# Performance work log

Hardware: AMD Instinct MI355X
Metric: run time of the kernel (lower is better)

## Reference

```python
import jax, jax.numpy as jnp
import numpy as np

N = 100000
E = 3200000
IN_DIM = 128
OUT_DIM = 64


def setup_inputs() -> dict:
    key = jax.random.key(0)
    k1, k2, k3, k4, k5, k6 = jax.random.split(key, 6)
    x = jax.random.normal(k1, (N, IN_DIM), dtype=jnp.float32)
    edge_index = jax.random.randint(k2, (2, E), 0, N, dtype=jnp.int64)
    edge_weight = jax.random.uniform(k3, (E,), dtype=jnp.float32)
    # Learned params: Linear weight (in->out, no bias), attention vectors a_src/a_tgt
    limit_w = float(np.sqrt(1.0 / IN_DIM))
    W = jax.random.uniform(k4, (IN_DIM, OUT_DIM), minval=-limit_w, maxval=limit_w, dtype=jnp.float32)
    # xavier_uniform for (out_dim, 1) parameters
    limit_a = float(np.sqrt(6.0 / (OUT_DIM + 1)))
    a_src = jax.random.uniform(k5, (OUT_DIM,), minval=-limit_a, maxval=limit_a, dtype=jnp.float32)
    a_tgt = jax.random.uniform(k6, (OUT_DIM,), minval=-limit_a, maxval=limit_a, dtype=jnp.float32)
    return {"x": x, "edge_index": edge_index, "edge_weight": edge_weight,
            "W": W, "a_src": a_src, "a_tgt": a_tgt}


def reference(x, edge_index, edge_weight, W, a_src, a_tgt):
    n = x.shape[0]
    h = x @ W  # (N, out_dim)
    src, tgt = edge_index[0], edge_index[1]
    # per-node attention logits, gathered per edge
    hs = h @ a_src  # (N,)
    ht = h @ a_tgt  # (N,)
    e = jax.nn.leaky_relu(hs[src] + ht[tgt], negative_slope=0.2)  # (E,)
    e = e * edge_weight
    # segment softmax over incoming edges of each target node
    e_max = jax.ops.segment_max(e, tgt, num_segments=n)  # (N,), -inf for isolated nodes
    e_exp = jnp.exp(e - e_max[tgt])  # (E,)
    e_sum = jax.ops.segment_sum(e_exp, tgt, num_segments=n)  # (N,)
    alpha = e_exp / (e_sum[tgt] + 1e-10)  # (E,)
    # weighted scatter-add aggregation
    out = jax.ops.segment_sum(alpha[:, None] * h[src], tgt, num_segments=n)  # (N, out_dim)
    return out
```

## Files before the change

kernel.cpp:

```cpp
#include <hip/hip_runtime.h>


#define IN_DIM 128
#define OUT_DIM 64
#define LNODES 64
#define MAXBKT 512
#define BKN 256
#define SEPT 8
#define SCHUNK (1024 * SEPT)
#define CAP 9216

__device__ __forceinline__ unsigned short f2bf(float f) {
    unsigned u = __float_as_uint(f);
    return (unsigned short)((u + 0x7FFFu + ((u >> 16) & 1u)) >> 16);
}
__device__ __forceinline__ float bf2f(unsigned short u) {
    return __uint_as_float((unsigned)u << 16);
}

__device__ __forceinline__ float expg(float d) {
    return __expf(fmaxf(d, -80.f));
}

__global__ __launch_bounds__(512) void k_linear(
    const float* __restrict__ x, const float* __restrict__ W,
    const float* __restrict__ a_src, const float* __restrict__ a_tgt,
    unsigned short* __restrict__ hh, float* __restrict__ hs,
    float* __restrict__ ht, int n)
{
    __shared__ float ws_W[IN_DIM][OUT_DIM];
    __shared__ float xs[LNODES][IN_DIM + 4];
    const int tid   = threadIdx.x;
    const int node0 = blockIdx.x * LNODES;

    {
        const float4* Wsrc = (const float4*)W;
        float4* Wdst = (float4*)&ws_W[0][0];
        #pragma unroll
        for (int i = 0; i < 4; ++i) Wdst[tid + 512 * i] = Wsrc[tid + 512 * i];
    }
    {
        int nrows = n - node0; if (nrows > LNODES) nrows = LNODES;
        for (int i = tid; i < nrows * 32; i += 512) {
            int r = i >> 5, c4 = i & 31;
            float4 v = ((const float4*)(x + (size_t)(node0 + r) * IN_DIM))[c4];
            *(float4*)&xs[r][c4 * 4] = v;
        }
    }
    __syncthreads();

    const int lane16 = tid & 15;
    const int mrow   = tid >> 4;
    float4 acc[2];
    acc[0] = make_float4(0.f, 0.f, 0.f, 0.f);
    acc[1] = make_float4(0.f, 0.f, 0.f, 0.f);

    #pragma unroll 2
    for (int k = 0; k < IN_DIM; k += 4) {
        float4 w0 = *(const float4*)&ws_W[k + 0][lane16 * 4];
        float4 w1 = *(const float4*)&ws_W[k + 1][lane16 * 4];
        float4 w2 = *(const float4*)&ws_W[k + 2][lane16 * 4];
        float4 w3 = *(const float4*)&ws_W[k + 3][lane16 * 4];
        #pragma unroll
        for (int u = 0; u < 2; ++u) {
            float4 xv = *(const float4*)&xs[mrow + 32 * u][k];
            acc[u].x += w0.x * xv.x + w1.x * xv.y + w2.x * xv.z + w3.x * xv.w;
            acc[u].y += w0.y * xv.x + w1.y * xv.y + w2.y * xv.z + w3.y * xv.w;
            acc[u].z += w0.z * xv.x + w1.z * xv.y + w2.z * xv.z + w3.z * xv.w;
            acc[u].w += w0.w * xv.x + w1.w * xv.y + w2.w * xv.z + w3.w * xv.w;
        }
    }

    const float4 as = ((const float4*)a_src)[lane16];
    const float4 at = ((const float4*)a_tgt)[lane16];
    #pragma unroll
    for (int u = 0; u < 2; ++u) {
        int node = node0 + mrow + 32 * u;
        float ps = acc[u].x * as.x + acc[u].y * as.y + acc[u].z * as.z + acc[u].w * as.w;
        float pt = acc[u].x * at.x + acc[u].y * at.y + acc[u].z * at.z + acc[u].w * at.w;
        #pragma unroll
        for (int off = 8; off; off >>= 1) {
            ps += __shfl_xor(ps, off);
            pt += __shfl_xor(pt, off);
        }
        if (node < n) {
            ushort4 hv;
            hv.x = f2bf(acc[u].x); hv.y = f2bf(acc[u].y);
            hv.z = f2bf(acc[u].z); hv.w = f2bf(acc[u].w);
            ((ushort4*)(hh + (size_t)node * OUT_DIM))[lane16] = hv;
            if (lane16 == 0) { hs[node] = ps; ht[node] = pt; }
        }
    }
}

__global__ __launch_bounds__(1024) void k_count(
    const int* __restrict__ tgt, int* __restrict__ histT,
    int ecount, int nbkt, int nsb)
{
    __shared__ int h[MAXBKT];
    const int tid = threadIdx.x;
    const int e0  = blockIdx.x * SCHUNK;
    for (int i = tid; i < nbkt; i += 1024) h[i] = 0;
    __syncthreads();
    #pragma unroll
    for (int k = 0; k < SEPT; ++k) {
        int j = e0 + k * 1024 + tid;
        if (j < ecount) atomicAdd(&h[tgt[j] >> 8], 1);
    }
    __syncthreads();
    for (int i = tid; i < nbkt; i += 1024) histT[i * nsb + blockIdx.x] = h[i];
}

__global__ __launch_bounds__(512) void k_colscan(
    int* __restrict__ histT, int* __restrict__ bfill, int nsb)
{
    __shared__ int lds[512];
    const int bkt = blockIdx.x;
    const int tid = threadIdx.x;
    int v = (tid < nsb) ? histT[bkt * nsb + tid] : 0;
    lds[tid] = v;
    __syncthreads();
    for (int off = 1; off < 512; off <<= 1) {
        int u = (tid >= off) ? lds[tid - off] : 0;
        __syncthreads();
        lds[tid] += u;
        __syncthreads();
    }
    int excl = lds[tid] - v;
    if (tid < nsb) histT[bkt * nsb + tid] = bkt * CAP + excl;
    if (tid == 511) bfill[bkt] = bkt * CAP + lds[511];
}

__global__ __launch_bounds__(1024) void k_scat(
    const int* __restrict__ src, const int* __restrict__ tgt,
    const float* __restrict__ ew, const float* __restrict__ hs,
    const float* __restrict__ ht, const int* __restrict__ histT,
    float2* __restrict__ ecoarse, int ecount, int nbkt, int nsb)
{
    __shared__ int h[MAXBKT];
    __shared__ int base[MAXBKT];
    const int tid = threadIdx.x;
    const int e0  = blockIdx.x * SCHUNK;

    for (int i = tid; i < nbkt; i += 1024) {
        h[i] = 0;
        base[i] = histT[i * nsb + blockIdx.x];
    }

    unsigned kreg[SEPT]; int breg[SEPT]; float wreg[SEPT];
    #pragma unroll
    for (int k = 0; k < SEPT; ++k) {
        int j = e0 + k * 1024 + tid;
        bool valid = j < ecount;
        int s = valid ? src[j] : 0;
        int t = valid ? tgt[j] : 0;
        wreg[k] = valid ? ew[j] : 0.f;
        kreg[k] = ((unsigned)s << 8) | ((unsigned)t & 255u);
        breg[k] = t >> 8;
    }
    float hsr[SEPT], htr[SEPT];
    #pragma unroll
    for (int k = 0; k < SEPT; ++k) hsr[k] = hs[kreg[k] >> 8];
    #pragma unroll
    for (int k = 0; k < SEPT; ++k) htr[k] = ht[(breg[k] << 8) | (int)(kreg[k] & 255u)];

    __syncthreads();

    int rank[SEPT];
    #pragma unroll
    for (int k = 0; k < SEPT; ++k) {
        int j = e0 + k * 1024 + tid;
        if (j < ecount) rank[k] = atomicAdd(&h[breg[k]], 1);
    }

    #pragma unroll
    for (int k = 0; k < SEPT; ++k) {
        int j = e0 + k * 1024 + tid;
        if (j < ecount) {
            float v = hsr[k] + htr[k];
            v = (v > 0.f) ? v : 0.2f * v;
            v *= wreg[k];
            ecoarse[base[breg[k]] + rank[k]] = make_float2(__uint_as_float(kreg[k]), v);
        }
    }
}

__global__ __launch_bounds__(1024, 8) void k_bucket(
    const int* __restrict__ bfill, const float2* __restrict__ ecoarse,
    const unsigned short* __restrict__ hh, float* __restrict__ out, int n)
{
    __shared__ float2 recs[CAP];
    __shared__ int   cnt[BKN];
    __shared__ int   pos0[BKN];
    __shared__ int   fill[BKN];
    __shared__ float mf[BKN];
    __shared__ float rden[BKN];

    const int tid   = threadIdx.x;
    const int bkt   = blockIdx.x;
    const int base  = bkt * CAP;
    const int node0 = bkt << 8;
    const int mcnt  = bfill[bkt] - base;

    for (int i = tid; i < BKN; i += 1024) cnt[i] = 0;
    __syncthreads();

    for (int j = tid; j < mcnt; j += 1024) {
        unsigned k = __float_as_uint(ecoarse[base + j].x);
        atomicAdd(&cnt[k & 255u], 1);
    }
    __syncthreads();

    if (tid < BKN) pos0[tid] = cnt[tid];
    __syncthreads();
    for (int off = 1; off < BKN; off <<= 1) {
        int u = 0;
        if (tid < BKN && tid >= off) u = pos0[tid - off];
        __syncthreads();
        if (tid < BKN) pos0[tid] += u;
        __syncthreads();
    }
    if (tid < BKN) fill[tid] = pos0[tid] - cnt[tid];
    __syncthreads();
    if (tid < BKN) pos0[tid] = fill[tid];
    __syncthreads();

    for (int j = tid; j < mcnt; j += 1024) {
        float2 e = ecoarse[base + j];
        unsigned k = __float_as_uint(e.x);
        int p = atomicAdd(&fill[k & 255u], 1);
        recs[p] = e;
    }
    __syncthreads();

    {
        const int G   = tid >> 4;
        const int l16 = tid & 15;
        #pragma unroll
        for (int r = 0; r < 4; ++r) {
            int tl = G + 64 * r;
            int s0 = pos0[tl], c = cnt[tl];
            float m = -INFINITY, s = 0.f;
            for (int j = l16; j < c; j += 16) {
                float v = recs[s0 + j].y;
                float nm = fmaxf(m, v);
                s = s * expg(m - nm) + expg(v - nm);
                m = nm;
            }
            #pragma unroll
            for (int off = 8; off; off >>= 1) {
                float mo = __shfl_xor(m, off);
                float so = __shfl_xor(s, off);
                float nm = fmaxf(m, mo);
                s = s * expg(m - nm) + so * expg(mo - nm);
                m = nm;
            }
            if (l16 == 0) { mf[tl] = m; rden[tl] = 1.f / (s + 1e-10f); }
        }
    }
    __syncthreads();

    const int lane = tid & 63;
    const int wv   = tid >> 6;
    const int g    = lane >> 4;
    const int l4   = lane & 15;
    #pragma unroll 1
    for (int r = 0; r < 16; ++r) {
        int tl = wv + 16 * r;
        int node = node0 + tl;
        if (node >= n) continue;
        int s0 = pos0[tl], e_ = s0 + cnt[tl];
        float m = mf[tl], rd = rden[tl];
        float4 a0 = make_float4(0.f, 0.f, 0.f, 0.f);
        float4 a1 = make_float4(0.f, 0.f, 0.f, 0.f);
        int j = s0;
        for (; j + 8 <= e_; j += 8) {
            float2 e0 = recs[j + g];
            float2 e1 = recs[j + 4 + g];
            int sA = (int)(__float_as_uint(e0.x) >> 8);
            int sB = (int)(__float_as_uint(e1.x) >> 8);
            ushort4 u0 = ((const ushort4*)(hh + (size_t)sA * OUT_DIM))[l4];
            ushort4 u1 = ((const ushort4*)(hh + (size_t)sB * OUT_DIM))[l4];
            float c0 = __expf(e0.y - m) * rd;
            float c1 = __expf(e1.y - m) * rd;
            a0.x += c0 * bf2f(u0.x); a0.y += c0 * bf2f(u0.y);
            a0.z += c0 * bf2f(u0.z); a0.w += c0 * bf2f(u0.w);
            a1.x += c1 * bf2f(u1.x); a1.y += c1 * bf2f(u1.y);
            a1.z += c1 * bf2f(u1.z); a1.w += c1 * bf2f(u1.w);
        }
        for (; j < e_; j += 4) {
            int jj = j + g;
            bool valid = jj < e_;
            float2 ed = recs[valid ? jj : (e_ - 1)];
            int sidx = (int)(__float_as_uint(ed.x) >> 8);
            ushort4 uv = ((const ushort4*)(hh + (size_t)sidx * OUT_DIM))[l4];
            float c = valid ? __expf(ed.y - m) * rd : 0.f;
            a0.x += c * bf2f(uv.x); a0.y += c * bf2f(uv.y);
            a0.z += c * bf2f(uv.z); a0.w += c * bf2f(uv.w);
        }
        a0.x += a1.x; a0.y += a1.y; a0.z += a1.z; a0.w += a1.w;

        #pragma unroll
        for (int off = 32; off >= 16; off >>= 1) {
            a0.x += __shfl_xor(a0.x, off);
            a0.y += __shfl_xor(a0.y, off);
            a0.z += __shfl_xor(a0.z, off);
            a0.w += __shfl_xor(a0.w, off);
        }
        if (g == 0)
            ((float4*)(out + (size_t)node * OUT_DIM))[l4] = a0;
    }
}

extern "C" void kernel_launch(void* const* d_in, const int* in_sizes, int n_in,
                              void* d_out, int out_size, void* d_ws, size_t ws_size,
                              hipStream_t stream) {
    const float* x     = (const float*)d_in[0];
    const int*   eidx  = (const int*)d_in[1];
    const float* ew    = (const float*)d_in[2];
    const float* W     = (const float*)d_in[3];
    const float* a_src = (const float*)d_in[4];
    const float* a_tgt = (const float*)d_in[5];
    float* out = (float*)d_out;

    const int n = in_sizes[0] / IN_DIM;
    const int E = in_sizes[2];
    const int* src = eidx;
    const int* tgt = eidx + E;
    const int nbkt = (n + BKN - 1) / BKN;
    const int nsb  = (E + SCHUNK - 1) / SCHUNK;

    unsigned* ws = (unsigned*)d_ws;
    unsigned short* hh = (unsigned short*)ws;  ws += (size_t)n * OUT_DIM / 2;
    float* hs     = (float*)ws;          ws += n;
    float* ht     = (float*)ws;          ws += n;
    int*   bfill  = (int*)ws;            ws += MAXBKT;
    int*   histT  = (int*)ws;            ws += (size_t)nbkt * nsb;
    ws = (unsigned*)(((uintptr_t)ws + 7) & ~(uintptr_t)7);
    float2* ecoarse = (float2*)ws;

    k_linear<<<(n + LNODES - 1) / LNODES, 512, 0, stream>>>(x, W, a_src, a_tgt, hh, hs, ht, n);
    k_count<<<nsb, 1024, 0, stream>>>(tgt, histT, E, nbkt, nsb);
    k_colscan<<<nbkt, 512, 0, stream>>>(histT, bfill, nsb);
    k_scat<<<nsb, 1024, 0, stream>>>(src, tgt, ew, hs, ht, histT, ecoarse, E, nbkt, nsb);
    k_bucket<<<nbkt, 1024, 0, stream>>>(bfill, ecoarse, hh, out, n);
}
```

Before: 271.6 us.

## Compute node linear projection with split-bf16 MFMA instead of scalar FP32 FMAs

Rewrites k_linear so x and W are split into bf16 hi/lo parts in shared memory. The product is then computed with three 16x16x32 bf16 MFMA instructions per tile (hi*hi, hi*lo, lo*hi), which approximates FP32 accuracy. The aim is to replace the scalar FMA loop with matrix-core throughput. It also stages the bf16 output through shared memory for coalesced stores. The extra cost is the hi/lo conversion work on every block, a transposed W layout in shared memory, and slightly lower precision than true FP32.

Result: no change. 271.3 us (-0.1%).

```diff
diff --git a/kernel.cpp b/kernel.cpp
--- a/kernel.cpp
+++ b/kernel.cpp
@@ -3,13 +3,15 @@
 
 #define IN_DIM 128
 #define OUT_DIM 64
-#define LNODES 64
 #define MAXBKT 512
 #define BKN 256
 #define SEPT 8
 #define SCHUNK (1024 * SEPT)
 #define CAP 9216
 
+typedef __attribute__((ext_vector_type(8))) short bf16x8;
+typedef __attribute__((ext_vector_type(4))) float f32x4;
+
 __device__ __forceinline__ unsigned short f2bf(float f) {
     unsigned u = __float_as_uint(f);
     return (unsigned short)((u + 0x7FFFu + ((u >> 16) & 1u)) >> 16);
@@ -22,73 +24,129 @@
     return __expf(fmaxf(d, -80.f));
 }
 
-__global__ __launch_bounds__(512) void k_linear(
+__global__ __launch_bounds__(256) void k_linear(
     const float* __restrict__ x, const float* __restrict__ W,
     const float* __restrict__ a_src, const float* __restrict__ a_tgt,
     unsigned short* __restrict__ hh, float* __restrict__ hs,
     float* __restrict__ ht, int n)
 {
-    __shared__ float ws_W[IN_DIM][OUT_DIM];
-    __shared__ float xs[LNODES][IN_DIM + 4];
+    __shared__ unsigned short xhi[64][136];
+    __shared__ unsigned short xlo[64][136];
+    __shared__ unsigned short whi[64][136];
+    __shared__ unsigned short wlo[64][136];
     const int tid   = threadIdx.x;
-    const int node0 = blockIdx.x * LNODES;
+    const int node0 = blockIdx.x * 64;
 
     {
-        const float4* Wsrc = (const float4*)W;
-        float4* Wdst = (float4*)&ws_W[0][0];
-        #pragma unroll
-        for (int i = 0; i < 4; ++i) Wdst[tid + 512 * i] = Wsrc[tid + 512 * i];
+        const float4* W4 = (const float4*)W;
+        #pragma unroll
+        for (int j = 0; j < 8; ++j) {
+            int i4 = tid + 256 * j;
+            int k = i4 >> 4, d4 = i4 & 15;
+            float4 v = W4[i4];
+            float vv[4] = {v.x, v.y, v.z, v.w};
+            #pragma unroll
+            for (int m = 0; m < 4; ++m) {
+                unsigned short hi = f2bf(vv[m]);
+                float lo = vv[m] - bf2f(hi);
+                whi[d4 * 4 + m][k] = hi;
+                wlo[d4 * 4 + m][k] = f2bf(lo);
+            }
+        }
     }
     {
-        int nrows = n - node0; if (nrows > LNODES) nrows = LNODES;
-        for (int i = tid; i < nrows * 32; i += 512) {
-            int r = i >> 5, c4 = i & 31;
-            float4 v = ((const float4*)(x + (size_t)(node0 + r) * IN_DIM))[c4];
-            *(float4*)&xs[r][c4 * 4] = v;
-        }
-    }
-    __syncthreads();
-
-    const int lane16 = tid & 15;
-    const int mrow   = tid >> 4;
-    float4 acc[2];
-    acc[0] = make_float4(0.f, 0.f, 0.f, 0.f);
-    acc[1] = make_float4(0.f, 0.f, 0.f, 0.f);
-
-    #pragma unroll 2
-    for (int k = 0; k < IN_DIM; k += 4) {
-        float4 w0 = *(const float4*)&ws_W[k + 0][lane16 * 4];
-        float4 w1 = *(const float4*)&ws_W[k + 1][lane16 * 4];
-        float4 w2 = *(const float4*)&ws_W[k + 2][lane16 * 4];
-        float4 w3 = *(const float4*)&ws_W[k + 3][lane16 * 4];
-        #pragma unroll
-        for (int u = 0; u < 2; ++u) {
-            float4 xv = *(const float4*)&xs[mrow + 32 * u][k];
-            acc[u].x += w0.x * xv.x + w1.x * xv.y + w2.x * xv.z + w3.x * xv.w;
-            acc[u].y += w0.y * xv.x + w1.y * xv.y + w2.y * xv.z + w3.y * xv.w;
-            acc[u].z += w0.z * xv.x + w1.z * xv.y + w2.z * xv.z + w3.z * xv.w;
-            acc[u].w += w0.w * xv.x + w1.w * xv.y + w2.w * xv.z + w3.w * xv.w;
-        }
-    }
-
-    const float4 as = ((const float4*)a_src)[lane16];
-    const float4 at = ((const float4*)a_tgt)[lane16];
-    #pragma unroll
-    for (int u = 0; u < 2; ++u) {
-        int node = node0 + mrow + 32 * u;
-        float ps = acc[u].x * as.x + acc[u].y * as.y + acc[u].z * as.z + acc[u].w * as.w;
-        float pt = acc[u].x * at.x + acc[u].y * at.y + acc[u].z * at.z + acc[u].w * at.w;
+        #pragma unroll
+        for (int j = 0; j < 8; ++j) {
+            int i4 = tid + 256 * j;
+            int r = i4 >> 5, c4 = i4 & 31;
+            int node = node0 + r;
+            float4 v = make_float4(0.f, 0.f, 0.f, 0.f);
+            if (node < n) v = ((const float4*)(x + (size_t)node * IN_DIM))[c4];
+            float vv[4] = {v.x, v.y, v.z, v.w};
+            ushort4 ph, pl;
+            unsigned short* php = (unsigned short*)&ph;
+            unsigned short* plp = (unsigned short*)&pl;
+            #pragma unroll
+            for (int m = 0; m < 4; ++m) {
+                unsigned short hi = f2bf(vv[m]);
+                php[m] = hi;
+                plp[m] = f2bf(vv[m] - bf2f(hi));
+            }
+            *(ushort4*)&xhi[r][c4 * 4] = ph;
+            *(ushort4*)&xlo[r][c4 * 4] = pl;
+        }
+    }
+    __syncthreads();
+
+    const int l15  = tid & 15;
+    const int lhi  = (tid & 63) >> 4;
+    const int wv   = tid >> 6;
+    const int arow = wv * 16 + l15;
+    const int kb   = lhi * 8;
+
+    bf16x8 ahi[4], alo[4];
+    #pragma unroll
+    for (int k0 = 0; k0 < 4; ++k0) {
+        ahi[k0] = *(const bf16x8*)&xhi[arow][k0 * 32 + kb];
+        alo[k0] = *(const bf16x8*)&xlo[arow][k0 * 32 + kb];
+    }
+
+    f32x4 acc[4];
+    #pragma unroll
+    for (int ntt = 0; ntt < 4; ++ntt) acc[ntt] = (f32x4){0.f, 0.f, 0.f, 0.f};
+
+    #pragma unroll
+    for (int ntt = 0; ntt < 4; ++ntt) {
+        #pragma unroll
+        for (int k0 = 0; k0 < 4; ++k0) {
+            bf16x8 bhi = *(const bf16x8*)&whi[ntt * 16 + l15][k0 * 32 + kb];
+            bf16x8 blo = *(const bf16x8*)&wlo[ntt * 16 + l15][k0 * 32 + kb];
+            acc[ntt] = __builtin_amdgcn_mfma_f32_16x16x32_bf16(ahi[k0], bhi, acc[ntt], 0, 0, 0);
+            acc[ntt] = __builtin_amdgcn_mfma_f32_16x16x32_bf16(ahi[k0], blo, acc[ntt], 0, 0, 0);
+            acc[ntt] = __builtin_amdgcn_mfma_f32_16x16x32_bf16(alo[k0], bhi, acc[ntt], 0, 0, 0);
+        }
+    }
+
+    float asv[4], atv[4];
+    #pragma unroll
+    for (int ntt = 0; ntt < 4; ++ntt) {
+        asv[ntt] = a_src[ntt * 16 + l15];
+        atv[ntt] = a_tgt[ntt * 16 + l15];
+    }
+    #pragma unroll
+    for (int q = 0; q < 4; ++q) {
+        float ps = 0.f, pt = 0.f;
+        #pragma unroll
+        for (int ntt = 0; ntt < 4; ++ntt) {
+            ps += acc[ntt][q] * asv[ntt];
+            pt += acc[ntt][q] * atv[ntt];
+        }
         #pragma unroll
         for (int off = 8; off; off >>= 1) {
             ps += __shfl_xor(ps, off);
             pt += __shfl_xor(pt, off);
         }
+        int node = node0 + wv * 16 + lhi * 4 + q;
+        if (l15 == 0 && node < n) { hs[node] = ps; ht[node] = pt; }
+    }
+
+    __syncthreads();
+    #pragma unroll
+    for (int ntt = 0; ntt < 4; ++ntt) {
+        #pragma unroll
+        for (int q = 0; q < 4; ++q) {
+            xhi[wv * 16 + lhi * 4 + q][ntt * 16 + l15] = f2bf(acc[ntt][q]);
+        }
+    }
+    __syncthreads();
+    #pragma unroll
+    for (int j = 0; j < 4; ++j) {
+        int i = tid + 256 * j;
+        int r = i >> 4, c4 = i & 15;
+        int node = node0 + r;
         if (node < n) {
-            ushort4 hv;
-            hv.x = f2bf(acc[u].x); hv.y = f2bf(acc[u].y);
-            hv.z = f2bf(acc[u].z); hv.w = f2bf(acc[u].w);
-            ((ushort4*)(hh + (size_t)node * OUT_DIM))[lane16] = hv;
-            if (lane16 == 0) { hs[node] = ps; ht[node] = pt; }
+            ushort4 v = *(const ushort4*)&xhi[r][c4 * 4];
+            ((ushort4*)(hh + (size_t)node * OUT_DIM))[c4] = v;
         }
     }
 }
@@ -339,7 +397,7 @@
     ws = (unsigned*)(((uintptr_t)ws + 7) & ~(uintptr_t)7);
     float2* ecoarse = (float2*)ws;
 
-    k_linear<<<(n + LNODES - 1) / LNODES, 512, 0, stream>>>(x, W, a_src, a_tgt, hh, hs, ht, n);
+    k_linear<<<(n + 63) / 64, 256, 0, stream>>>(x, W, a_src, a_tgt, hh, hs, ht, n);
     k_count<<<nsb, 1024, 0, stream>>>(tgt, histT, E, nbkt, nsb);
     k_colscan<<<nbkt, 512, 0, stream>>>(histT, bfill, nsb);
     k_scat<<<nsb, 1024, 0, stream>>>(src, tgt, ew, hs, ht, histT, ecoarse, E, nbkt, nsb);
```
